# Performance work log

Measured on AMD Instinct MI355X. Metric: run time of the kernel, lower is better.

The kernel has to match this reference:

```python
import jax, jax.numpy as jnp
import numpy as np

# Config constants (match init_kwargs)
N_EXPERTS = 8
CAPACITY = 1280
W_IMPORTANCE = 0.01
W_LOAD = 0.01
LAMBDA_Z = 0.001
W_PENALTY = 0.01


def setup_inputs() -> dict:
    key = jax.random.key(0)
    ks = jax.random.split(key, 6)
    B, T, C, E, F = 4, 2048, 1024, N_EXPERTS, 4096
    s = 0.02
    return {
        "x": jax.random.normal(ks[0], (B, T, C), dtype=jnp.float32),
        "gate_w": jax.random.normal(ks[1], (E, C), dtype=jnp.float32) * s,
        "gate_b": jnp.zeros((E,), dtype=jnp.float32),
        "w1": jax.random.normal(ks[2], (E, F, C), dtype=jnp.float32) * s,
        "b1": jnp.zeros((E, F), dtype=jnp.float32),
        "w2": jax.random.normal(ks[3], (E, C, F), dtype=jnp.float32) * s,
        "b2": jnp.zeros((E, C), dtype=jnp.float32),
    }


def reference(x, gate_w, gate_b, w1, b1, w2, b2):
    B, T, C = x.shape
    E = N_EXPERTS
    xf = x.reshape(B * T, C)
    bt = xf.shape[0]

    # ---- routing ----
    gate_logits = xf @ gate_w.T + gate_b  # (BT, E)

    # penalty loss
    p = jax.nn.softmax(gate_logits / 1.66, axis=-1)
    pen_a = jnp.mean(p * (1.0 - p))
    pm = p.mean(axis=0)
    pen_b = 1.0 / E - jnp.mean(pm * (1.0 - pm))
    penalty = W_PENALTY * (pen_a + pen_b)

    # z-loss
    z_loss = LAMBDA_Z * jnp.mean(jax.nn.logsumexp(gate_logits, axis=-1) ** 2)

    router_probs = jax.nn.softmax(gate_logits.astype(jnp.float32), axis=-1).astype(x.dtype)
    top1_idx = jnp.argmax(router_probs, axis=-1)        # (BT,)
    top1_w = jnp.max(router_probs, axis=-1)             # (BT,)
    onehot = jax.nn.one_hot(top1_idx, E, dtype=jnp.int32)

    # capacity masking: position of each token within its chosen expert
    priority = jnp.cumsum(onehot, axis=0)               # (BT, E)
    pos = priority[jnp.arange(bt), top1_idx] - 1        # (BT,)
    keep = pos < CAPACITY                               # (BT,) bool

    # load-balance loss
    f_i = onehot.astype(x.dtype).mean(axis=0)
    P_i = router_probs.mean(axis=0)
    load_loss = W_LOAD * E * jnp.sum(f_i * P_i)

    # importance loss (scatter of top1 probs == onehot-weighted sum)
    importance = (onehot.astype(x.dtype) * top1_w[:, None]).sum(axis=0)  # (E,)
    cv2 = jnp.var(importance) / jnp.mean(importance) ** 2
    importance_loss = W_IMPORTANCE * cv2

    aux_loss = penalty + z_loss + load_loss + importance_loss

    # ---- dispatch -> grouped FFN -> combine ----
    pos_c = jnp.clip(pos, 0, CAPACITY - 1)
    keep_f = keep.astype(x.dtype)[:, None]
    buf = jnp.zeros((E, CAPACITY, C), dtype=x.dtype).at[top1_idx, pos_c].add(xf * keep_f)
    h = jax.nn.gelu(jnp.einsum('ekc,efc->ekf', buf, w1) + b1[:, None, :], approximate=True)
    yb = jnp.einsum('ekf,ecf->ekc', h, w2) + b2[:, None, :]
    y = yb[top1_idx, pos_c] * keep_f                    # dropped tokens -> 0

    out = (top1_w[:, None] * y).reshape(B, T, C)
    return out, aux_loss
```

## Files before the change

### kernel.cpp

```cpp
#include <hip/hip_runtime.h>
#include <hip/hip_bf16.h>
#include <stdint.h>

#define BTOK 8192
#define CDIM 1024
#define NEXP 8
#define FDIM 4096
#define ECAP 1280

typedef __attribute__((ext_vector_type(8))) unsigned short u16x8;
typedef __attribute__((ext_vector_type(8))) __bf16 bf16x8;
typedef __attribute__((ext_vector_type(4))) float f32x4;

__device__ __forceinline__ unsigned short f2bf(float f) {
    unsigned int u = __builtin_bit_cast(unsigned int, f);
    u += 0x7FFFu + ((u >> 16) & 1u);
    return (unsigned short)(u >> 16);
}

__device__ __forceinline__ bf16x8 lds_load8(const unsigned short* p) {
    return __builtin_bit_cast(bf16x8, *(const u16x8*)p);
}

__device__ __forceinline__ float gelu_tanh(float v) {
    float u = 0.7978845608028654f * (v + 0.044715f * v * v * v);
    float e = __expf(2.0f * u);
    float t = 1.0f - 2.0f * __builtin_amdgcn_rcpf(e + 1.0f);
    return 0.5f * v * (1.0f + t);
}

__global__ __launch_bounds__(256) void cvt_kernel(
    const float* __restrict__ src, unsigned short* __restrict__ dst, int n8)
{
    int i = blockIdx.x * 256 + threadIdx.x;
    if (i >= n8) return;
    const float4* s = (const float4*)(src + (size_t)i * 8);
    float4 a = s[0], b = s[1];
    u16x8 o;
    o[0] = f2bf(a.x); o[1] = f2bf(a.y); o[2] = f2bf(a.z); o[3] = f2bf(a.w);
    o[4] = f2bf(b.x); o[5] = f2bf(b.y); o[6] = f2bf(b.z); o[7] = f2bf(b.w);
    *(u16x8*)(dst + (size_t)i * 8) = o;
}

__global__ __launch_bounds__(256) void gate_kernel(
    const float* __restrict__ x,
    const float* __restrict__ gw,
    const float* __restrict__ gb,
    float* __restrict__ logits)
{
    const int lane = threadIdx.x & 63;
    const int wave = threadIdx.x >> 6;
    const int tok = blockIdx.x * 4 + wave;
    const float* xr = x + (size_t)tok * CDIM + lane * 16;
    float xv[16];
#pragma unroll
    for (int j = 0; j < 4; j++) {
        float4 v = ((const float4*)xr)[j];
        xv[4 * j] = v.x; xv[4 * j + 1] = v.y; xv[4 * j + 2] = v.z; xv[4 * j + 3] = v.w;
    }
    float acc[8];
#pragma unroll
    for (int e = 0; e < 8; e++) {
        const float* wr = gw + e * CDIM + lane * 16;
        float s = 0.f;
#pragma unroll
        for (int j = 0; j < 4; j++) {
            float4 v = ((const float4*)wr)[j];
            s += xv[4 * j] * v.x + xv[4 * j + 1] * v.y + xv[4 * j + 2] * v.z + xv[4 * j + 3] * v.w;
        }
        acc[e] = s;
    }
#pragma unroll
    for (int e = 0; e < 8; e++) {
#pragma unroll
        for (int off = 32; off > 0; off >>= 1)
            acc[e] += __shfl_xor(acc[e], off);
    }
    if (lane == 0) {
#pragma unroll
        for (int e = 0; e < 8; e++)
            logits[(size_t)tok * 8 + e] = acc[e] + gb[e];
    }
}

__global__ __launch_bounds__(256) void route_kernel(
    const float* __restrict__ logits,
    int* __restrict__ top1i, float* __restrict__ top1w,
    int* __restrict__ toks, float* __restrict__ slotw,
    int* __restrict__ cnt, float* __restrict__ aux_out)
{
    const int tid = threadIdx.x;
    const int TPT = BTOK / 256;
    float psum[8] = {}, qsum[8] = {}, imp[8] = {};
    int cnte[8] = {};
    float pen_a_s = 0.f, z_s = 0.f;
    const float INV_T = 1.0f / 1.66f;

    for (int i = 0; i < TPT; i++) {
        int t = tid * TPT + i;
        float l[8];
#pragma unroll
        for (int e = 0; e < 8; e++) l[e] = logits[t * 8 + e];
        float m = l[0];
#pragma unroll
        for (int e = 1; e < 8; e++) m = fmaxf(m, l[e]);
        float ex[8], se = 0.f;
#pragma unroll
        for (int e = 0; e < 8; e++) { ex[e] = __expf(l[e] - m); se += ex[e]; }
        float inv = 1.0f / se;
#pragma unroll
        for (int e = 0; e < 8; e++) psum[e] += ex[e] * inv;
        int am = 0; float bl = l[0];
#pragma unroll
        for (int e = 1; e < 8; e++) if (l[e] > bl) { bl = l[e]; am = e; }
        float w = ex[am] * inv;
        imp[am] += w; cnte[am]++;
        top1i[t] = am; top1w[t] = w;
        float lse = m + __logf(se);
        z_s += lse * lse;
        float m2 = m * INV_T, se2 = 0.f, ex2[8];
#pragma unroll
        for (int e = 0; e < 8; e++) { ex2[e] = __expf(l[e] * INV_T - m2); se2 += ex2[e]; }
        float inv2 = 1.0f / se2;
#pragma unroll
        for (int e = 0; e < 8; e++) { float q = ex2[e] * inv2; pen_a_s += q * (1.f - q); qsum[e] += q; }
    }

    __shared__ int sc[256][8];
#pragma unroll
    for (int e = 0; e < 8; e++) sc[tid][e] = cnte[e];
    __syncthreads();
    for (int st = 1; st < 256; st <<= 1) {
        int v[8];
        bool act = (tid >= st);
        if (act) {
#pragma unroll
            for (int e = 0; e < 8; e++) v[e] = sc[tid - st][e];
        }
        __syncthreads();
        if (act) {
#pragma unroll
            for (int e = 0; e < 8; e++) sc[tid][e] += v[e];
        }
        __syncthreads();
    }
    int run[8], tot[8];
#pragma unroll
    for (int e = 0; e < 8; e++) {
        run[e] = (tid > 0) ? sc[tid - 1][e] : 0;
        tot[e] = sc[255][e];
    }
    for (int i = 0; i < TPT; i++) {
        int t = tid * TPT + i;
        int am = top1i[t];
        int pos = 0;
#pragma unroll
        for (int e = 0; e < 8; e++) if (e == am) pos = run[e]++;
        if (pos < ECAP) {
            toks[am * ECAP + pos] = t;
            slotw[am * ECAP + pos] = top1w[t];
        }
    }
    if (tid < 8) cnt[tid] = (tot[tid] < ECAP) ? tot[tid] : ECAP;

    __shared__ float red[26][256];
    red[0][tid] = pen_a_s;
    red[1][tid] = z_s;
#pragma unroll
    for (int e = 0; e < 8; e++) {
        red[2 + e][tid] = qsum[e];
        red[10 + e][tid] = psum[e];
        red[18 + e][tid] = imp[e];
    }
    __syncthreads();
    for (int st = 128; st > 0; st >>= 1) {
        if (tid < st) {
#pragma unroll
            for (int j = 0; j < 26; j++) red[j][tid] += red[j][tid + st];
        }
        __syncthreads();
    }
    if (tid == 0) {
        const float BTf = (float)BTOK;
        float pen_a = red[0][0] / (BTf * 8.f);
        float pb = 0.f;
        for (int e = 0; e < 8; e++) { float pm = red[2 + e][0] / BTf; pb += pm * (1.f - pm); }
        float pen_b = 0.125f - pb * 0.125f;
        float penalty = 0.01f * (pen_a + pen_b);
        float z = 0.001f * red[1][0] / BTf;
        float load = 0.f;
        for (int e = 0; e < 8; e++) load += ((float)tot[e] / BTf) * (red[10 + e][0] / BTf);
        load *= 0.01f * 8.f;
        float mu = 0.f;
        for (int e = 0; e < 8; e++) mu += red[18 + e][0];
        mu *= 0.125f;
        float var = 0.f;
        for (int e = 0; e < 8; e++) { float d = red[18 + e][0] - mu; var += d * d; }
        var *= 0.125f;
        float cv2 = var / (mu * mu);
        float aux = penalty + z + load + 0.01f * cv2;
        aux_out[0] = aux;
    }
}

__global__ __launch_bounds__(256) void ffn1_kernel(
    const unsigned short* __restrict__ xb,
    const unsigned short* __restrict__ w1b,
    const float* __restrict__ b1,
    const int* __restrict__ toks,
    const int* __restrict__ cnt,
    unsigned short* __restrict__ H)
{
    const int e = blockIdx.y;
    const int MT = ECAP / 128;
    const int mt = blockIdx.x % MT;
    const int nt = blockIdx.x / MT;
    const int cnt_e = cnt[e];
    const int m0 = mt * 128;
    if (m0 >= cnt_e) return;
    const int n0 = nt * 128;
    const unsigned short* W = w1b + (size_t)e * FDIM * CDIM;
    const int* tk = toks + e * ECAP;

    __shared__ __align__(16) unsigned short As[128 * 64];
    __shared__ __align__(16) unsigned short Bs[128 * 64];

    const int tid = threadIdx.x;
    const int lane = tid & 63;
    const int wave = tid >> 6;
    const int wm = wave & 1;
    const int wn = wave >> 1;

    const unsigned short* gA[4];
    const unsigned short* gB[4];
    unsigned short* lA[4];
    unsigned short* lB[4];
#pragma unroll
    for (int j = 0; j < 4; j++) {
        int idx = j * 256 + tid;
        int r = idx >> 3, ch = idx & 7;
        int row = m0 + r;
        int tokid = (row < cnt_e) ? tk[row] : 0;
        if ((unsigned)tokid >= BTOK) tokid = 0;
        gA[j] = xb + (size_t)tokid * CDIM + ch * 8;
        gB[j] = W + (size_t)(n0 + r) * CDIM + ch * 8;
        lA[j] = As + idx * 8;
        lB[j] = Bs + idx * 8;
    }
    f32x4 acc[4][4] = {};
    const int fr = lane & 15;
    const int kq = (lane >> 4) * 8;
    for (int k0 = 0; k0 < CDIM; k0 += 64) {
        u16x8 va[4], vb[4];
#pragma unroll
        for (int j = 0; j < 4; j++) {
            va[j] = *(const u16x8*)(gA[j] + k0);
            vb[j] = *(const u16x8*)(gB[j] + k0);
        }
        __syncthreads();
#pragma unroll
        for (int j = 0; j < 4; j++) {
            *(u16x8*)lA[j] = va[j];
            *(u16x8*)lB[j] = vb[j];
        }
        __syncthreads();
#pragma unroll
        for (int kk = 0; kk < 64; kk += 32) {
            bf16x8 af[4], bfr[4];
#pragma unroll
            for (int i = 0; i < 4; i++) {
                af[i]  = lds_load8(&As[(wm * 64 + i * 16 + fr) * 64 + kk + kq]);
                bfr[i] = lds_load8(&Bs[(wn * 64 + i * 16 + fr) * 64 + kk + kq]);
            }
#pragma unroll
            for (int i = 0; i < 4; i++)
#pragma unroll
                for (int j = 0; j < 4; j++)
                    acc[i][j] = __builtin_amdgcn_mfma_f32_16x16x32_bf16(af[i], bfr[j], acc[i][j], 0, 0, 0);
        }
    }
    const int cq = (lane >> 4) * 4;
#pragma unroll
    for (int i = 0; i < 4; i++) {
#pragma unroll
        for (int j = 0; j < 4; j++) {
            int n = n0 + wn * 64 + j * 16 + fr;
            float bias = b1[e * FDIM + n];
            size_t base = ((size_t)e * ECAP + (m0 + wm * 64 + i * 16 + cq)) * FDIM + n;
#pragma unroll
            for (int rr = 0; rr < 4; rr++) {
                float v = acc[i][j][rr] + bias;
                H[base + (size_t)rr * FDIM] = f2bf(gelu_tanh(v));
            }
        }
    }
}

__global__ __launch_bounds__(256) void ffn2_kernel(
    const unsigned short* __restrict__ H,
    const unsigned short* __restrict__ w2b,
    const float* __restrict__ b2,
    const int* __restrict__ toks,
    const float* __restrict__ slotw,
    const int* __restrict__ cnt,
    float* __restrict__ out)
{
    const int e = blockIdx.y;
    const int MT = ECAP / 128;
    const int mt = blockIdx.x % MT;
    const int nt = blockIdx.x / MT;
    const int cnt_e = cnt[e];
    const int m0 = mt * 128;
    if (m0 >= cnt_e) return;
    const int n0 = nt * 128;
    const unsigned short* W = w2b + (size_t)e * CDIM * FDIM;
    const unsigned short* Hb = H + (size_t)e * ECAP * FDIM;

    __shared__ __align__(16) unsigned short As[128 * 64];
    __shared__ __align__(16) unsigned short Bs[128 * 64];

    const int tid = threadIdx.x;
    const int lane = tid & 63;
    const int wave = tid >> 6;
    const int wm = wave & 1;
    const int wn = wave >> 1;

    const unsigned short* gA[4];
    const unsigned short* gB[4];
    unsigned short* lA[4];
    unsigned short* lB[4];
#pragma unroll
    for (int j = 0; j < 4; j++) {
        int idx = j * 256 + tid;
        int r = idx >> 3, ch = idx & 7;
        gA[j] = Hb + (size_t)(m0 + r) * FDIM + ch * 8;
        gB[j] = W + (size_t)(n0 + r) * FDIM + ch * 8;
        lA[j] = As + idx * 8;
        lB[j] = Bs + idx * 8;
    }
    f32x4 acc[4][4] = {};
    const int fr = lane & 15;
    const int kq = (lane >> 4) * 8;
    for (int k0 = 0; k0 < FDIM; k0 += 64) {
        u16x8 va[4], vb[4];
#pragma unroll
        for (int j = 0; j < 4; j++) {
            va[j] = *(const u16x8*)(gA[j] + k0);
            vb[j] = *(const u16x8*)(gB[j] + k0);
        }
        __syncthreads();
#pragma unroll
        for (int j = 0; j < 4; j++) {
            *(u16x8*)lA[j] = va[j];
            *(u16x8*)lB[j] = vb[j];
        }
        __syncthreads();
#pragma unroll
        for (int kk = 0; kk < 64; kk += 32) {
            bf16x8 af[4], bfr[4];
#pragma unroll
            for (int i = 0; i < 4; i++) {
                af[i]  = lds_load8(&As[(wm * 64 + i * 16 + fr) * 64 + kk + kq]);
                bfr[i] = lds_load8(&Bs[(wn * 64 + i * 16 + fr) * 64 + kk + kq]);
            }
#pragma unroll
            for (int i = 0; i < 4; i++)
#pragma unroll
                for (int j = 0; j < 4; j++)
                    acc[i][j] = __builtin_amdgcn_mfma_f32_16x16x32_bf16(af[i], bfr[j], acc[i][j], 0, 0, 0);
        }
    }
    const int cq = (lane >> 4) * 4;
#pragma unroll
    for (int i = 0; i < 4; i++) {
#pragma unroll
        for (int rr = 0; rr < 4; rr++) {
            int s = m0 + wm * 64 + i * 16 + cq + rr;
            if (s < cnt_e) {
                int t = toks[e * ECAP + s];
                float wgt = slotw[e * ECAP + s];
                if ((unsigned)t < BTOK) {
#pragma unroll
                    for (int j = 0; j < 4; j++) {
                        int n = n0 + wn * 64 + j * 16 + fr;
                        float y = acc[i][j][rr] + b2[e * CDIM + n];
                        out[(size_t)t * CDIM + n] = wgt * y;
                    }
                }
            }
        }
    }
}

extern "C" void kernel_launch(void* const* d_in, const int* in_sizes, int n_in,
                              void* d_out, int out_size, void* d_ws, size_t ws_size,
                              hipStream_t stream)
{
    (void)in_sizes; (void)n_in; (void)ws_size;
    const float* x  = (const float*)d_in[0];
    const float* gw = (const float*)d_in[1];
    const float* gb = (const float*)d_in[2];
    const float* w1 = (const float*)d_in[3];
    const float* b1 = (const float*)d_in[4];
    const float* w2 = (const float*)d_in[5];
    const float* b2 = (const float*)d_in[6];
    float* out = (float*)d_out;

    char* ws = (char*)d_ws;
    size_t off = 0;
    unsigned short* H   = (unsigned short*)(ws + off); off += (size_t)NEXP * ECAP * FDIM * 2;
    unsigned short* xb  = (unsigned short*)(ws + off); off += (size_t)BTOK * CDIM * 2;
    unsigned short* w1b = (unsigned short*)(ws + off); off += (size_t)NEXP * FDIM * CDIM * 2;
    unsigned short* w2b = (unsigned short*)(ws + off); off += (size_t)NEXP * CDIM * FDIM * 2;
    float* logits = (float*)(ws + off); off += (size_t)BTOK * 8 * 4;
    int* top1i    = (int*)(ws + off);   off += (size_t)BTOK * 4;
    float* top1w  = (float*)(ws + off); off += (size_t)BTOK * 4;
    int* toks     = (int*)(ws + off);   off += (size_t)NEXP * ECAP * 4;
    float* slotw  = (float*)(ws + off); off += (size_t)NEXP * ECAP * 4;
    int* cnt      = (int*)(ws + off);   off += (size_t)NEXP * 4;

    hipMemsetAsync(d_out, 0, (size_t)out_size * sizeof(float), stream);

    const int NX = BTOK * CDIM / 8;
    const int NW = NEXP * FDIM * CDIM / 8;
    cvt_kernel<<<(NX + 255) / 256, 256, 0, stream>>>(x, xb, NX);
    cvt_kernel<<<(NW + 255) / 256, 256, 0, stream>>>(w1, w1b, NW);
    cvt_kernel<<<(NW + 255) / 256, 256, 0, stream>>>(w2, w2b, NW);

    gate_kernel<<<BTOK / 4, 256, 0, stream>>>(x, gw, gb, logits);
    route_kernel<<<1, 256, 0, stream>>>(logits, top1i, top1w, toks, slotw, cnt,
                                        out + (size_t)BTOK * CDIM);
    ffn1_kernel<<<dim3((ECAP / 128) * (FDIM / 128), NEXP), 256, 0, stream>>>(xb, w1b, b1, toks, cnt, H);
    ffn2_kernel<<<dim3((ECAP / 128) * (CDIM / 128), NEXP), 256, 0, stream>>>(H, w2b, b2, toks, slotw, cnt, out);
}
```

Measured before the change: 766.6 us.

## Load GEMM tiles directly to LDS with XOR swizzle and remap block order

Both FFN GEMM kernels now stage A and B tiles with global_load_lds (direct global-to-LDS 16-byte loads) instead of going through registers. The global addresses are XOR-swizzled so reads from LDS avoid bank conflicts. Block indices are also permuted in strides of 8, which changes how tiles are spread across XCDs and cache. This saves VGPRs and instruction overhead, but there is still no double buffering, so every iteration now pays two barriers.

```diff
diff --git a/kernel.cpp b/kernel.cpp
--- a/kernel.cpp
+++ b/kernel.cpp
@@ -27,6 +27,13 @@
     float e = __expf(2.0f * u);
     float t = 1.0f - 2.0f * __builtin_amdgcn_rcpf(e + 1.0f);
     return 0.5f * v * (1.0f + t);
+}
+
+__device__ __forceinline__ void glds16(const unsigned short* g, unsigned short* l) {
+    __builtin_amdgcn_global_load_lds(
+        (const __attribute__((address_space(1))) void*)g,
+        (__attribute__((address_space(3))) void*)l,
+        16, 0, 0);
 }
 
 __global__ __launch_bounds__(256) void cvt_kernel(
@@ -213,8 +220,11 @@
 {
     const int e = blockIdx.y;
     const int MT = ECAP / 128;
-    const int mt = blockIdx.x % MT;
-    const int nt = blockIdx.x / MT;
+    const int nbq = (int)gridDim.x >> 3;
+    const int bid = blockIdx.x;
+    const int b2 = (bid & 7) * nbq + (bid >> 3);
+    const int mt = b2 % MT;
+    const int nt = b2 / MT;
     const int cnt_e = cnt[e];
     const int m0 = mt * 128;
     if (m0 >= cnt_e) return;
@@ -230,38 +240,30 @@
     const int wave = tid >> 6;
     const int wm = wave & 1;
     const int wn = wave >> 1;
+    const int wbase = wave * 512;
 
     const unsigned short* gA[4];
     const unsigned short* gB[4];
-    unsigned short* lA[4];
-    unsigned short* lB[4];
 #pragma unroll
     for (int j = 0; j < 4; j++) {
         int idx = j * 256 + tid;
-        int r = idx >> 3, ch = idx & 7;
+        int r = idx >> 3;
+        int ch = (idx & 7) ^ (r & 7);
         int row = m0 + r;
         int tokid = (row < cnt_e) ? tk[row] : 0;
         if ((unsigned)tokid >= BTOK) tokid = 0;
         gA[j] = xb + (size_t)tokid * CDIM + ch * 8;
         gB[j] = W + (size_t)(n0 + r) * CDIM + ch * 8;
-        lA[j] = As + idx * 8;
-        lB[j] = Bs + idx * 8;
     }
     f32x4 acc[4][4] = {};
     const int fr = lane & 15;
     const int kq = (lane >> 4) * 8;
+    const int sw = (fr & 7) << 3;
     for (int k0 = 0; k0 < CDIM; k0 += 64) {
-        u16x8 va[4], vb[4];
 #pragma unroll
         for (int j = 0; j < 4; j++) {
-            va[j] = *(const u16x8*)(gA[j] + k0);
-            vb[j] = *(const u16x8*)(gB[j] + k0);
-        }
-        __syncthreads();
-#pragma unroll
-        for (int j = 0; j < 4; j++) {
-            *(u16x8*)lA[j] = va[j];
-            *(u16x8*)lB[j] = vb[j];
+            glds16(gA[j] + k0, As + j * 2048 + wbase);
+            glds16(gB[j] + k0, Bs + j * 2048 + wbase);
         }
         __syncthreads();
 #pragma unroll
@@ -269,8 +271,8 @@
             bf16x8 af[4], bfr[4];
 #pragma unroll
             for (int i = 0; i < 4; i++) {
-                af[i]  = lds_load8(&As[(wm * 64 + i * 16 + fr) * 64 + kk + kq]);
-                bfr[i] = lds_load8(&Bs[(wn * 64 + i * 16 + fr) * 64 + kk + kq]);
+                af[i]  = lds_load8(&As[(wm * 64 + i * 16 + fr) * 64 + ((kk + kq) ^ sw)]);
+                bfr[i] = lds_load8(&Bs[(wn * 64 + i * 16 + fr) * 64 + ((kk + kq) ^ sw)]);
             }
 #pragma unroll
             for (int i = 0; i < 4; i++)
@@ -278,6 +280,7 @@
                 for (int j = 0; j < 4; j++)
                     acc[i][j] = __builtin_amdgcn_mfma_f32_16x16x32_bf16(af[i], bfr[j], acc[i][j], 0, 0, 0);
         }
+        __syncthreads();
     }
     const int cq = (lane >> 4) * 4;
 #pragma unroll
@@ -307,8 +310,11 @@
 {
     const int e = blockIdx.y;
     const int MT = ECAP / 128;
-    const int mt = blockIdx.x % MT;
-    const int nt = blockIdx.x / MT;
+    const int nbq = (int)gridDim.x >> 3;
+    const int bid = blockIdx.x;
+    const int b2i = (bid & 7) * nbq + (bid >> 3);
+    const int mt = b2i % MT;
+    const int nt = b2i / MT;
     const int cnt_e = cnt[e];
     const int m0 = mt * 128;
     if (m0 >= cnt_e) return;
@@ -324,35 +330,27 @@
     const int wave = tid >> 6;
     const int wm = wave & 1;
     const int wn = wave >> 1;
+    const int wbase = wave * 512;
 
     const unsigned short* gA[4];
     const unsigned short* gB[4];
-    unsigned short* lA[4];
-    unsigned short* lB[4];
 #pragma unroll
     for (int j = 0; j < 4; j++) {
         int idx = j * 256 + tid;
-        int r = idx >> 3, ch = idx & 7;
+        int r = idx >> 3;
+        int ch = (idx & 7) ^ (r & 7);
         gA[j] = Hb + (size_t)(m0 + r) * FDIM + ch * 8;
         gB[j] = W + (size_t)(n0 + r) * FDIM + ch * 8;
-        lA[j] = As + idx * 8;
-        lB[j] = Bs + idx * 8;
     }
     f32x4 acc[4][4] = {};
     const int fr = lane & 15;
     const int kq = (lane >> 4) * 8;
+    const int sw = (fr & 7) << 3;
     for (int k0 = 0; k0 < FDIM; k0 += 64) {
-        u16x8 va[4], vb[4];
 #pragma unroll
         for (int j = 0; j < 4; j++) {
-            va[j] = *(const u16x8*)(gA[j] + k0);
-            vb[j] = *(const u16x8*)(gB[j] + k0);
-        }
-        __syncthreads();
-#pragma unroll
-        for (int j = 0; j < 4; j++) {
-            *(u16x8*)lA[j] = va[j];
-            *(u16x8*)lB[j] = vb[j];
+            glds16(gA[j] + k0, As + j * 2048 + wbase);
+            glds16(gB[j] + k0, Bs + j * 2048 + wbase);
         }
         __syncthreads();
 #pragma unroll
@@ -360,8 +358,8 @@
             bf16x8 af[4], bfr[4];
 #pragma unroll
             for (int i = 0; i < 4; i++) {
-                af[i]  = lds_load8(&As[(wm * 64 + i * 16 + fr) * 64 + kk + kq]);
-                bfr[i] = lds_load8(&Bs[(wn * 64 + i * 16 + fr) * 64 + kk + kq]);
+                af[i]  = lds_load8(&As[(wm * 64 + i * 16 + fr) * 64 + ((kk + kq) ^ sw)]);
+                bfr[i] = lds_load8(&Bs[(wn * 64 + i * 16 + fr) * 64 + ((kk + kq) ^ sw)]);
             }
 #pragma unroll
             for (int i = 0; i < 4; i++)
@@ -369,6 +367,7 @@
                 for (int j = 0; j < 4; j++)
                     acc[i][j] = __builtin_amdgcn_mfma_f32_16x16x32_bf16(af[i], bfr[j], acc[i][j], 0, 0, 0);
         }
+        __syncthreads();
     }
     const int cq = (lane >> 4) * 4;
 #pragma unroll
```

Result: faster. 711.9 us (-7.1%).
